# Optimization experiments

Hardware: AMD Instinct MI355X
Metric: run time of the kernel (lower is better)

## Reference

```python
import jax, jax.numpy as jnp
import numpy as np

N = 10000      # nodes
E = 320000     # edges
IN = 256       # in_dim == out_dim
H = 8          # heads
D = 32         # head_dim = in_dim // heads
CLAMP = 5.0
BN_EPS = 1e-5


def setup_inputs() -> dict:
    key = jax.random.key(0)
    ks = jax.random.split(key, 24)
    s = 0.05
    nrm = lambda k, shape, sc=s: (jax.random.normal(k, shape, jnp.float32) * sc)
    inp = {
        "x": nrm(ks[0], (N, IN), 1.0),
        "edge_attr": nrm(ks[1], (E, IN), 1.0),
        "log_deg": jax.random.uniform(ks[2], (N, 1), jnp.float32, 0.1, 3.0),
        "edge_index": jax.random.randint(ks[3], (2, E), 0, N, jnp.int32),
        # attention projections (stored [in, out]; x @ W + b)
        "Qw": nrm(ks[4], (IN, H * D)), "Qb": jnp.zeros((H * D,), jnp.float32),
        "Kw": nrm(ks[5], (IN, H * D)), "Kb": jnp.zeros((H * D,), jnp.float32),
        "Ew": nrm(ks[6], (IN, H * D * 2)), "Eb": jnp.zeros((H * D * 2,), jnp.float32),
        "Vw": nrm(ks[7], (IN, H * D)), "Vb": jnp.zeros((H * D,), jnp.float32),
        "Aw": nrm(ks[8], (D, H, 1)),
        "VeRow": nrm(ks[9], (D, H, D)),
        # layer params
        "deg_coef": nrm(ks[10], (1, H * D, 2)),
        "Now": nrm(ks[11], (H * D, IN)), "Nob": jnp.zeros((IN,), jnp.float32),
        "Eow": nrm(ks[12], (H * D, IN)), "Eob": jnp.zeros((IN,), jnp.float32),
        "bn1n_g": jnp.ones((IN,), jnp.float32), "bn1n_b": jnp.zeros((IN,), jnp.float32),
        "bn1e_g": jnp.ones((IN,), jnp.float32), "bn1e_b": jnp.zeros((IN,), jnp.float32),
        "f1w": nrm(ks[13], (IN, 2 * IN)), "f1b": jnp.zeros((2 * IN,), jnp.float32),
        "f2w": nrm(ks[14], (2 * IN, IN)), "f2b": jnp.zeros((IN,), jnp.float32),
        "bn2_g": jnp.ones((IN,), jnp.float32), "bn2_b": jnp.zeros((IN,), jnp.float32),
    }
    return inp


def _bn(x, g, b):
    # batch_norm with batch statistics (bn_no_runner=True => track_running_stats=False)
    mu = jnp.mean(x, axis=0)
    var = jnp.mean(jnp.square(x - mu), axis=0)  # biased, as torch BN
    return (x - mu) * jax.lax.rsqrt(var + BN_EPS) * g + b


def _attention(x, edge_attr, edge_index, Qw, Qb, Kw, Kb, Ew, Eb, Vw, Vb, Aw, VeRow):
    n = x.shape[0]
    src, dst = edge_index[0], edge_index[1]
    Qh = (x @ Qw + Qb).reshape(n, H, D)
    Kh = (x @ Kw + Kb).reshape(n, H, D)
    Vh = (x @ Vw + Vb).reshape(n, H, D)
    Ex = (edge_attr @ Ew + Eb).reshape(-1, H, 2 * D)
    score1 = Kh[src] + Qh[dst]                      # [E,H,D]
    s2 = Ex[:, :, :D] * Ex[:, :, D:]
    score2 = jnp.sign(s2) * jnp.sqrt(jnp.abs(s2))   # == sqrt(relu(s2)) - sqrt(relu(-s2))
    conn = jax.nn.relu(score1 + score2)             # [E,H,D] (attn act='relu')
    score = jnp.einsum('ehd,dhc->ehc', conn, Aw)    # [E,H,1]
    score = jnp.clip(score, -CLAMP, CLAMP)
    # segment softmax over destination nodes
    m = jax.ops.segment_max(score, dst, num_segments=n)
    e = jnp.exp(score - m[dst])
    ssum = jax.ops.segment_sum(e, dst, num_segments=n)
    attn = e / (ssum[dst] + 1e-16)                  # [E,H,1]
    msg = Vh[src] * attn
    Vo = Qh + jax.ops.segment_sum(msg, dst, num_segments=n)
    rowV = jax.ops.segment_sum(conn * attn, dst, num_segments=n)
    rowV = jnp.einsum('nhd,dhc->nhc', rowV, VeRow)
    Vo = Vo + rowV
    return Vo.reshape(n, H * D), conn.reshape(-1, H * D)


def reference(x, edge_attr, log_deg, edge_index, Qw, Qb, Kw, Kb, Ew, Eb, Vw, Vb,
              Aw, VeRow, deg_coef, Now, Nob, Eow, Eob, bn1n_g, bn1n_b,
              bn1e_g, bn1e_b, f1w, f1b, f2w, f2b, bn2_g, bn2_b):
    nh, eh = _attention(x, edge_attr, edge_index, Qw, Qb, Kw, Kb, Ew, Eb, Vw, Vb, Aw, VeRow)
    # degree scaler
    nh = nh * deg_coef[:, :, 0] + (nh * log_deg) * deg_coef[:, :, 1]
    nh = nh @ Now + Nob
    eh = eh @ Eow + Eob
    nh = x + nh
    eh = edge_attr + eh
    nh = _bn(nh, bn1n_g, bn1n_b)
    eh = _bn(eh, bn1e_g, bn1e_b)
    ffn = jax.nn.relu(nh @ f1w + f1b) @ f2w + f2b
    nh = _bn(nh + ffn, bn2_g, bn2_b)
    return nh, eh
```

## Files before the change

### kernel.cpp

```cpp
#include <hip/hip_runtime.h>

#define NN 10000
#define NE 320000

typedef float f4 __attribute__((ext_vector_type(4)));
typedef float f32x4 __attribute__((ext_vector_type(4)));
typedef short bf16x8 __attribute__((ext_vector_type(8)));

__device__ __forceinline__ unsigned short f2b(float f) {
  unsigned u = __float_as_uint(f);
  u += 0x7fff + ((u >> 16) & 1);
  return (unsigned short)(u >> 16);
}
__device__ __forceinline__ float b2f(unsigned short s) {
  return __uint_as_float(((unsigned)s) << 16);
}
__device__ __forceinline__ bf16x8 pack8(f4 a, f4 b) {
  bf16x8 r;
  r[0] = (short)f2b(a[0]); r[1] = (short)f2b(a[1]);
  r[2] = (short)f2b(a[2]); r[3] = (short)f2b(a[3]);
  r[4] = (short)f2b(b[0]); r[5] = (short)f2b(b[1]);
  r[6] = (short)f2b(b[2]); r[7] = (short)f2b(b[3]);
  return r;
}
__device__ __forceinline__ int swz(int row, int k) {
  return (row * 256) + (k ^ ((row & 7) << 3));
}

__global__ void castw_k(const float* __restrict__ in, unsigned short* __restrict__ out,
                        int K, int lg)
{
  int idx = blockIdx.x * 256 + threadIdx.x;
  if (idx >= (K << lg)) return;
  int n = idx & ((1 << lg) - 1), k = idx >> lg;
  out[(size_t)n * K + k] = f2b(in[idx]);
}

__global__ void cat3_k(const float* __restrict__ a, const float* __restrict__ b,
                       const float* __restrict__ c, float* __restrict__ o)
{
  int t = threadIdx.x;
  o[t] = a[t]; o[256 + t] = b[t]; o[512 + t] = c[t];
}

__global__ __launch_bounds__(256) void gemm_bf16_k(
    const float* __restrict__ A, const unsigned short* __restrict__ BT,
    const float* __restrict__ bias, const float* __restrict__ res,
    float* __restrict__ C, float* __restrict__ stats,
    int M, int K, int NT, int flags)
{
  __shared__ unsigned short Al[64][40];
  __shared__ unsigned short Bl[128][40];
  const int t = threadIdx.x;
  const int n0 = blockIdx.x * 128;
  const int m0 = blockIdx.y * 64;
  const int lane = t & 63, c = lane & 15, g = lane >> 4, w = t >> 6;
  f32x4 acc[8] = {};
  for (int k0 = 0; k0 < K; k0 += 32) {
    {
      int row = t >> 2, kk = (t & 3) * 8;
      f4 v0 = {0.f,0.f,0.f,0.f}, v1 = {0.f,0.f,0.f,0.f};
      if (m0 + row < M) {
        const f4* p = (const f4*)(A + (size_t)(m0 + row) * K + k0 + kk);
        v0 = p[0]; v1 = p[1];
      }
      __syncthreads();
      *(bf16x8*)&Al[row][kk] = pack8(v0, v1);
    }
    {
      int col = t >> 1, kk = (t & 1) * 16;
      const bf16x8* p = (const bf16x8*)(BT + (size_t)(n0 + col) * K + k0 + kk);
      *(bf16x8*)&Bl[col][kk] = p[0];
      *(bf16x8*)&Bl[col][kk + 8] = p[1];
    }
    __syncthreads();
    bf16x8 a = *(bf16x8*)&Al[w * 16 + c][g * 8];
#pragma unroll
    for (int nb = 0; nb < 8; nb++) {
      bf16x8 b = *(bf16x8*)&Bl[nb * 16 + c][g * 8];
      acc[nb] = __builtin_amdgcn_mfma_f32_16x16x32_bf16(a, b, acc[nb], 0, 0, 0);
    }
  }
  const int do_relu = flags & 1, do_stats = flags & 2;
#pragma unroll
  for (int nb = 0; nb < 8; nb++) {
    const int col = n0 + nb * 16 + c;
    const float bs = bias[col];
    float sn = 0.f, qn = 0.f;
#pragma unroll
    for (int r = 0; r < 4; r++) {
      int row = m0 + w * 16 + g * 4 + r;
      if (row < M) {
        float v = acc[nb][r] + bs;
        if (res) v += res[(size_t)row * NT + col];
        if (do_relu) v = fmaxf(v, 0.f);
        C[(size_t)row * NT + col] = v;
        sn += v; qn += v * v;
      }
    }
    if (do_stats) {
      sn += __shfl_xor(sn, 16); sn += __shfl_xor(sn, 32);
      qn += __shfl_xor(qn, 16); qn += __shfl_xor(qn, 32);
      if (g == 0) {
        atomicAdd(&stats[col], sn);
        atomicAdd(&stats[NT + col], qn);
      }
    }
  }
}

__global__ __launch_bounds__(256) void edge_conn_k(
    const float* __restrict__ EA, const unsigned short* __restrict__ EwT,
    const float* __restrict__ Eb, const float* __restrict__ QKVh,
    const int* __restrict__ ei, const float* __restrict__ Aw,
    float* __restrict__ connf, unsigned short* __restrict__ connb,
    float* __restrict__ score, int CB)
{
  __shared__ unsigned short Abuf[16384];
  __shared__ unsigned short Bbuf[16384];
  float* Exl = (float*)Bbuf;
  const int t = threadIdx.x;
  const int e0 = blockIdx.x * 64;
  const int lane = t & 63, c = lane & 15, g = lane >> 4, w = t >> 6;
#pragma unroll
  for (int it = 0; it < 8; it++) {
    int o = t + it * 256;
    int row = o >> 5, kk = (o & 31) * 8;
    const f4* p = (const f4*)(EA + (size_t)(e0 + row) * 256 + kk);
    f4 v0 = p[0], v1 = p[1];
    *(bf16x8*)&Abuf[swz(row, kk)] = pack8(v0, v1);
  }
  const int m2 = t >> 2, dg = t & 3;
  const int e = e0 + m2;
  const int src = ei[e], dst = ei[NE + e];
  for (int h = 0; h < 8; h++) {
    __syncthreads();
#pragma unroll
    for (int it = 0; it < 8; it++) {
      int o = t + it * 256;
      int row = o >> 5, kk = (o & 31) * 8;
      *(bf16x8*)&Bbuf[swz(row, kk)] =
          *(const bf16x8*)(EwT + (size_t)(h * 64 + row) * 256 + kk);
    }
    __syncthreads();
    f32x4 acc[4] = {};
#pragma unroll
    for (int ks = 0; ks < 8; ks++) {
      bf16x8 a = *(bf16x8*)&Abuf[swz(w * 16 + c, ks * 32 + g * 8)];
#pragma unroll
      for (int cb = 0; cb < 4; cb++) {
        bf16x8 b = *(bf16x8*)&Bbuf[swz(cb * 16 + c, ks * 32 + g * 8)];
        acc[cb] = __builtin_amdgcn_mfma_f32_16x16x32_bf16(a, b, acc[cb], 0, 0, 0);
      }
    }
    __syncthreads();
#pragma unroll
    for (int cb = 0; cb < 4; cb++) {
      float eb = Eb[h * 64 + cb * 16 + c];
#pragma unroll
      for (int r = 0; r < 4; r++)
        Exl[(w * 16 + g * 4 + r) * 68 + cb * 16 + c] = acc[cb][r] + eb;
    }
    __syncthreads();
    const int cb2 = h * 32 + dg * 8;
    const float* ex = Exl + m2 * 68;
    f4 x1a = *(const f4*)(ex + dg * 8);
    f4 x1b = *(const f4*)(ex + dg * 8 + 4);
    f4 x2a = *(const f4*)(ex + 32 + dg * 8);
    f4 x2b = *(const f4*)(ex + 32 + dg * 8 + 4);
    f4 k1 = *(const f4*)(QKVh + (size_t)src * 768 + 256 + cb2);
    f4 k2 = *(const f4*)(QKVh + (size_t)src * 768 + 256 + cb2 + 4);
    f4 q1 = *(const f4*)(QKVh + (size_t)dst * 768 + cb2);
    f4 q2 = *(const f4*)(QKVh + (size_t)dst * 768 + cb2 + 4);
    f4 c1, c2;
    float part = 0.f;
#pragma unroll
    for (int j = 0; j < 4; j++) {
      float s2 = x1a[j] * x2a[j];
      float v = copysignf(sqrtf(fabsf(s2)), s2) + k1[j] + q1[j];
      v = fmaxf(v, 0.f);
      c1[j] = v;
      part += v * Aw[(dg * 8 + j) * 8 + h];
      float s2b = x1b[j] * x2b[j];
      float vb = copysignf(sqrtf(fabsf(s2b)), s2b) + k2[j] + q2[j];
      vb = fmaxf(vb, 0.f);
      c2[j] = vb;
      part += vb * Aw[(dg * 8 + 4 + j) * 8 + h];
    }
    if (CB) {
      *(bf16x8*)(connb + (size_t)e * 256 + cb2) = pack8(c1, c2);
    } else {
      *(f4*)(connf + (size_t)e * 256 + cb2) = c1;
      *(f4*)(connf + (size_t)e * 256 + cb2 + 4) = c2;
    }
    part += __shfl_xor(part, 1);
    part += __shfl_xor(part, 2);
    if (dg == 0) score[(size_t)e * 8 + h] = fminf(fmaxf(part, -5.f), 5.f);
  }
}

__global__ void hist_k(const int* __restrict__ ei, int* __restrict__ cnt)
{
  int e = blockIdx.x * 256 + threadIdx.x;
  if (e < NE) atomicAdd(&cnt[ei[NE + e]], 1);
}

__global__ __launch_bounds__(256) void scan_k(const int* __restrict__ cnt, int* __restrict__ off)
{
  __shared__ int part[256];
  const int t = threadIdx.x;
  const int PER = 40;
  const int base = t * PER;
  int s = 0;
  for (int i = 0; i < PER; i++) {
    int b = base + i;
    if (b < NN) s += cnt[b];
  }
  part[t] = s;
  __syncthreads();
  for (int d = 1; d < 256; d <<= 1) {
    int v = (t >= d) ? part[t - d] : 0;
    __syncthreads();
    part[t] += v;
    __syncthreads();
  }
  int run = (t == 0) ? 0 : part[t - 1];
  for (int i = 0; i < PER; i++) {
    int b = base + i;
    if (b < NN) { off[b] = run; run += cnt[b]; }
  }
  if (t == 255) off[NN] = run;
}

__global__ void scat_k(const int* __restrict__ ei, const int* __restrict__ off,
                       int* __restrict__ cur, int* __restrict__ elist,
                       int* __restrict__ src_s)
{
  int e = blockIdx.x * 256 + threadIdx.x;
  if (e < NE) {
    int s = ei[e], d = ei[NE + e];
    int p = atomicAdd(&cur[d], 1);
    int j = off[d] + p;
    elist[j] = e;
    src_s[j] = s;
  }
}

__global__ __launch_bounds__(256) void node_agg_k(
    const int* __restrict__ off, const int* __restrict__ elist,
    const int* __restrict__ src_s, const float* __restrict__ score,
    const float* __restrict__ QKVh, const float* __restrict__ connf,
    const unsigned short* __restrict__ connb, int CB,
    const float* __restrict__ VeRow, const float* __restrict__ deg_coef,
    const float* __restrict__ log_deg, float* __restrict__ nh_a)
{
  const int n = blockIdx.x, t = threadIdx.x;
  const int h = t >> 5;
  __shared__ int eL[128];
  __shared__ int srcL[128];
  __shared__ float sS[1024];
  __shared__ float mS[8];
  __shared__ float rA[256];
  const int start = off[n];
  const int deg = off[n + 1] - start;
  float m = -1e30f, ssum = 0.f, vo = 0.f, ro = 0.f;
  for (int c0 = 0; c0 < deg; c0 += 128) {
    const int cn = min(128, deg - c0);
    __syncthreads();
    if (t < cn) {
      int jj = start + c0 + t;
      eL[t] = elist[jj];
      srcL[t] = src_s[jj];
    }
    __syncthreads();
    for (int i = t; i < cn * 8; i += 256) sS[i] = score[(size_t)eL[i >> 3] * 8 + (i & 7)];
    __syncthreads();
    float mc = -1e30f;
    for (int i = (t & 31); i < cn; i += 32) mc = fmaxf(mc, sS[i * 8 + h]);
    mc = fmaxf(mc, __shfl_xor(mc, 1));
    mc = fmaxf(mc, __shfl_xor(mc, 2));
    mc = fmaxf(mc, __shfl_xor(mc, 4));
    mc = fmaxf(mc, __shfl_xor(mc, 8));
    mc = fmaxf(mc, __shfl_xor(mc, 16));
    float nm = fmaxf(m, mc);
    if ((t & 31) == 0) mS[h] = nm;
    __syncthreads();
    for (int i = t; i < cn * 8; i += 256) sS[i] = __expf(sS[i] - mS[i & 7]);
    __syncthreads();
    float sc = __expf(m - nm);
    ssum *= sc; vo *= sc; ro *= sc;
    m = nm;
    int i = 0;
    if (CB) {
      for (; i + 4 <= cn; i += 4) {
        float w0 = sS[(i + 0) * 8 + h], w1 = sS[(i + 1) * 8 + h];
        float w2 = sS[(i + 2) * 8 + h], w3 = sS[(i + 3) * 8 + h];
        int s0 = srcL[i], s1 = srcL[i + 1], s2 = srcL[i + 2], s3 = srcL[i + 3];
        int f0 = eL[i], f1 = eL[i + 1], f2 = eL[i + 2], f3 = eL[i + 3];
        ssum += w0 + w1 + w2 + w3;
        vo = fmaf(w0, QKVh[(size_t)s0 * 768 + 512 + t], vo);
        vo = fmaf(w1, QKVh[(size_t)s1 * 768 + 512 + t], vo);
        vo = fmaf(w2, QKVh[(size_t)s2 * 768 + 512 + t], vo);
        vo = fmaf(w3, QKVh[(size_t)s3 * 768 + 512 + t], vo);
        ro = fmaf(w0, b2f(connb[(size_t)f0 * 256 + t]), ro);
        ro = fmaf(w1, b2f(connb[(size_t)f1 * 256 + t]), ro);
        ro = fmaf(w2, b2f(connb[(size_t)f2 * 256 + t]), ro);
        ro = fmaf(w3, b2f(connb[(size_t)f3 * 256 + t]), ro);
      }
      for (; i < cn; i++) {
        float w0 = sS[i * 8 + h];
        ssum += w0;
        vo = fmaf(w0, QKVh[(size_t)srcL[i] * 768 + 512 + t], vo);
        ro = fmaf(w0, b2f(connb[(size_t)eL[i] * 256 + t]), ro);
      }
    } else {
      for (; i + 4 <= cn; i += 4) {
        float w0 = sS[(i + 0) * 8 + h], w1 = sS[(i + 1) * 8 + h];
        float w2 = sS[(i + 2) * 8 + h], w3 = sS[(i + 3) * 8 + h];
        int s0 = srcL[i], s1 = srcL[i + 1], s2 = srcL[i + 2], s3 = srcL[i + 3];
        int f0 = eL[i], f1 = eL[i + 1], f2 = eL[i + 2], f3 = eL[i + 3];
        ssum += w0 + w1 + w2 + w3;
        vo = fmaf(w0, QKVh[(size_t)s0 * 768 + 512 + t], vo);
        vo = fmaf(w1, QKVh[(size_t)s1 * 768 + 512 + t], vo);
        vo = fmaf(w2, QKVh[(size_t)s2 * 768 + 512 + t], vo);
        vo = fmaf(w3, QKVh[(size_t)s3 * 768 + 512 + t], vo);
        ro = fmaf(w0, connf[(size_t)f0 * 256 + t], ro);
        ro = fmaf(w1, connf[(size_t)f1 * 256 + t], ro);
        ro = fmaf(w2, connf[(size_t)f2 * 256 + t], ro);
        ro = fmaf(w3, connf[(size_t)f3 * 256 + t], ro);
      }
      for (; i < cn; i++) {
        float w0 = sS[i * 8 + h];
        ssum += w0;
        vo = fmaf(w0, QKVh[(size_t)srcL[i] * 768 + 512 + t], vo);
        ro = fmaf(w0, connf[(size_t)eL[i] * 256 + t], ro);
      }
    }
  }
  const float inv = 1.f / (ssum + 1e-16f);
  vo *= inv;
  ro *= inv;
  __syncthreads();
  rA[t] = ro;
  __syncthreads();
  float acc = 0.f;
#pragma unroll
  for (int d = 0; d < 32; d++) acc = fmaf(rA[h * 32 + d], VeRow[d * 256 + t], acc);
  float v = QKVh[(size_t)n * 768 + t] + vo + acc;
  const float ld = log_deg[n];
  v = v * (deg_coef[2 * t] + ld * deg_coef[2 * t + 1]);
  nh_a[(size_t)n * 256 + t] = v;
}

__global__ __launch_bounds__(256) void eh_gemm_k(
    const unsigned short* __restrict__ EowT, const float* __restrict__ Eob,
    const float* __restrict__ EA, const unsigned short* __restrict__ connb, int CB,
    float* __restrict__ eh, float* __restrict__ stb)
{
  __shared__ unsigned short Al[64][264];
  __shared__ unsigned short Bl[256][40];
  __shared__ float lsum[256], lsq[256];
  const int t = threadIdx.x;
  const int e0 = blockIdx.x * 64;
  const int lane = t & 63, c = lane & 15, g = lane >> 4, w = t >> 6;
  lsum[t] = 0.f; lsq[t] = 0.f;
#pragma unroll
  for (int it = 0; it < 8; it++) {
    int o = t + it * 256;
    int row = o >> 5, kk = (o & 31) * 8;
    if (CB) {
      *(bf16x8*)&Al[row][kk] = *(const bf16x8*)(connb + (size_t)(e0 + row) * 256 + kk);
    } else {
      const f4* p = (const f4*)(eh + (size_t)(e0 + row) * 256 + kk);
      f4 v0 = p[0], v1 = p[1];
      *(bf16x8*)&Al[row][kk] = pack8(v0, v1);
    }
  }
  f32x4 acc[16] = {};
  for (int ks = 0; ks < 8; ks++) {
    __syncthreads();
#pragma unroll
    for (int it = 0; it < 4; it++) {
      int o = t + it * 256;
      int row = o >> 2, kk = (o & 3) * 8;
      *(bf16x8*)&Bl[row][kk] = *(const bf16x8*)(EowT + (size_t)row * 256 + ks * 32 + kk);
    }
    __syncthreads();
    bf16x8 a = *(bf16x8*)&Al[w * 16 + c][ks * 32 + g * 8];
#pragma unroll
    for (int nb = 0; nb < 16; nb++) {
      bf16x8 b = *(bf16x8*)&Bl[nb * 16 + c][g * 8];
      acc[nb] = __builtin_amdgcn_mfma_f32_16x16x32_bf16(a, b, acc[nb], 0, 0, 0);
    }
  }
#pragma unroll
  for (int nb = 0; nb < 16; nb++) {
    const int col = nb * 16 + c;
    const float eob = Eob[col];
    float sn = 0.f, qn = 0.f;
#pragma unroll
    for (int r = 0; r < 4; r++) {
      size_t row = e0 + w * 16 + g * 4 + r;
      float v = acc[nb][r] + eob + EA[row * 256 + col];
      eh[row * 256 + col] = v;
      sn += v; qn += v * v;
    }
    sn += __shfl_xor(sn, 16); sn += __shfl_xor(sn, 32);
    qn += __shfl_xor(qn, 16); qn += __shfl_xor(qn, 32);
    if (g == 0) { atomicAdd(&lsum[col], sn); atomicAdd(&lsq[col], qn); }
  }
  __syncthreads();
  float* dstb = stb + (size_t)(blockIdx.x & 63) * 512;
  atomicAdd(&dstb[t], lsum[t]);
  atomicAdd(&dstb[256 + t], lsq[t]);
}

__global__ void bn_fin_k(float* __restrict__ st, float invR)
{
  int t = threadIdx.x;
  float mean = st[t] * invR;
  float var = st[256 + t] * invR - mean * mean;
  st[t] = mean;
  st[256 + t] = rsqrtf(var + 1e-5f);
}

__global__ void bn_fin_banked_k(const float* __restrict__ banks, float* __restrict__ st,
                                float invR)
{
  int t = threadIdx.x;
  float s = 0.f, q = 0.f;
  for (int b = 0; b < 64; b++) {
    s += banks[(size_t)b * 512 + t];
    q += banks[(size_t)b * 512 + 256 + t];
  }
  float mean = s * invR;
  float var = q * invR - mean * mean;
  st[t] = mean;
  st[256 + t] = rsqrtf(var + 1e-5f);
}

__global__ void bn_apply_k(const float* __restrict__ X, float* __restrict__ Y,
                           const float* __restrict__ st, const float* __restrict__ g,
                           const float* __restrict__ b, long nvec)
{
  long i = (long)blockIdx.x * 256 + threadIdx.x;
  if (i >= nvec) return;
  int base = (int)(i & 63) * 4;
  f4 x = *(const f4*)(X + i * 4);
  f4 mn = *(const f4*)(st + base);
  f4 rs = *(const f4*)(st + 256 + base);
  f4 gg = *(const f4*)(g + base);
  f4 bb = *(const f4*)(b + base);
  f4 y;
#pragma unroll
  for (int j = 0; j < 4; j++) y[j] = (x[j] - mn[j]) * rs[j] * gg[j] + bb[j];
  *(f4*)(Y + i * 4) = y;
}

extern "C" void kernel_launch(void* const* d_in, const int* in_sizes, int n_in,
                              void* d_out, int out_size, void* d_ws, size_t ws_size,
                              hipStream_t stream)
{
  (void)in_sizes; (void)n_in; (void)out_size;
  const float* x        = (const float*)d_in[0];
  const float* edge_attr= (const float*)d_in[1];
  const float* log_deg  = (const float*)d_in[2];
  const int*   ei       = (const int*)d_in[3];
  const float* Qw = (const float*)d_in[4];  const float* Qb = (const float*)d_in[5];
  const float* Kw = (const float*)d_in[6];  const float* Kb = (const float*)d_in[7];
  const float* Ew = (const float*)d_in[8];  const float* Eb = (const float*)d_in[9];
  const float* Vw = (const float*)d_in[10]; const float* Vb = (const float*)d_in[11];
  const float* Aw = (const float*)d_in[12]; const float* VeRow = (const float*)d_in[13];
  const float* deg_coef = (const float*)d_in[14];
  const float* Now = (const float*)d_in[15]; const float* Nob = (const float*)d_in[16];
  const float* Eow = (const float*)d_in[17]; const float* Eob = (const float*)d_in[18];
  const float* bn1n_g = (const float*)d_in[19]; const float* bn1n_b = (const float*)d_in[20];
  const float* bn1e_g = (const float*)d_in[21]; const float* bn1e_b = (const float*)d_in[22];
  const float* f1w = (const float*)d_in[23]; const float* f1b = (const float*)d_in[24];
  const float* f2w = (const float*)d_in[25]; const float* f2b = (const float*)d_in[26];
  const float* bn2_g = (const float*)d_in[27]; const float* bn2_b = (const float*)d_in[28];

  float* out_nh = (float*)d_out;
  float* out_eh = out_nh + (size_t)NN * 256;

  float* ws     = (float*)d_ws;
  float* QKVh   = ws;
  float* score  = QKVh + (size_t)NN * 768;
  float* nh_a   = score + 2560000;
  float* nh2    = nh_a + 2560000;
  float* ffn1   = nh2 + 2560000;
  float* st1    = ffn1 + 5120000;
  float* st2    = st1 + 512;
  float* st3    = st2 + 512;
  float* stb    = st3 + 512;
  float* biasQKV= stb + 64 * 512;
  unsigned short* QwT = (unsigned short*)(biasQKV + 768);
  unsigned short* KwT = QwT + 65536;
  unsigned short* VwT = KwT + 65536;
  unsigned short* NowT= VwT + 65536;
  unsigned short* EowT= NowT + 65536;
  unsigned short* EwT = EowT + 65536;
  unsigned short* f1wT= EwT + 131072;
  unsigned short* f2wT= f1wT + 131072;
  int*   cnt    = (int*)(f2wT + 131072);
  int*   off    = cnt + NN;
  int*   cur    = off + NN + 1;
  int*   elist  = cur + NN;
  int*   src_s  = elist + NE;
  unsigned short* connb = (unsigned short*)(src_s + NE);
  size_t need = (size_t)((char*)(connb + (size_t)NE * 256) - (char*)d_ws);
  const int CB = (ws_size >= need) ? 1 : 0;

  hipMemsetAsync(cnt, 0, (size_t)NN * 4, stream);
  hipMemsetAsync(cur, 0, (size_t)NN * 4, stream);
  hipMemsetAsync(st1, 0, (size_t)2 * 512 * 4, stream);
  hipMemsetAsync(stb, 0, (size_t)64 * 512 * 4, stream);

  dim3 blk(256);

  castw_k<<<dim3(256), blk, 0, stream>>>(Qw, QwT, 256, 8);
  castw_k<<<dim3(256), blk, 0, stream>>>(Kw, KwT, 256, 8);
  castw_k<<<dim3(256), blk, 0, stream>>>(Vw, VwT, 256, 8);
  castw_k<<<dim3(256), blk, 0, stream>>>(Now, NowT, 256, 8);
  castw_k<<<dim3(256), blk, 0, stream>>>(Eow, EowT, 256, 8);
  castw_k<<<dim3(512), blk, 0, stream>>>(Ew, EwT, 256, 9);
  castw_k<<<dim3(512), blk, 0, stream>>>(f1w, f1wT, 256, 9);
  castw_k<<<dim3(512), blk, 0, stream>>>(f2w, f2wT, 512, 8);
  cat3_k<<<dim3(1), blk, 0, stream>>>(Qb, Kb, Vb, biasQKV);

  hist_k<<<dim3(NE / 256), blk, 0, stream>>>(ei, cnt);
  scan_k<<<dim3(1), blk, 0, stream>>>(cnt, off);
  scat_k<<<dim3(NE / 256), blk, 0, stream>>>(ei, off, cur, elist, src_s);

  gemm_bf16_k<<<dim3(6, 157), blk, 0, stream>>>(x, QwT, biasQKV, nullptr, QKVh, nullptr,
                                                NN, 256, 768, 0);

  edge_conn_k<<<dim3(NE / 64), blk, 0, stream>>>(edge_attr, EwT, Eb, QKVh, ei, Aw,
                                                 out_eh, connb, score, CB);

  node_agg_k<<<dim3(NN), blk, 0, stream>>>(off, elist, src_s, score, QKVh,
                                           out_eh, connb, CB,
                                           VeRow, deg_coef, log_deg, nh_a);

  eh_gemm_k<<<dim3(NE / 64), blk, 0, stream>>>(EowT, Eob, edge_attr, connb, CB,
                                               out_eh, stb);
  bn_fin_banked_k<<<dim3(1), blk, 0, stream>>>(stb, st3, 1.0f / NE);
  bn_apply_k<<<dim3(NE * 64 / 256), blk, 0, stream>>>(out_eh, out_eh, st3,
                                                      bn1e_g, bn1e_b, (long)NE * 64);

  gemm_bf16_k<<<dim3(2, 157), blk, 0, stream>>>(nh_a, NowT, Nob, x, out_nh, st1,
                                                NN, 256, 256, 2);
  bn_fin_k<<<dim3(1), blk, 0, stream>>>(st1, 1.0f / NN);
  bn_apply_k<<<dim3(NN * 64 / 256), blk, 0, stream>>>(out_nh, nh2, st1,
                                                      bn1n_g, bn1n_b, (long)NN * 64);
  gemm_bf16_k<<<dim3(4, 157), blk, 0, stream>>>(nh2, f1wT, f1b, nullptr, ffn1, nullptr,
                                                NN, 256, 512, 1);
  gemm_bf16_k<<<dim3(2, 157), blk, 0, stream>>>(ffn1, f2wT, f2b, nh2, out_nh, st2,
                                                NN, 512, 256, 2);
  bn_fin_k<<<dim3(1), blk, 0, stream>>>(st2, 1.0f / NN);
  bn_apply_k<<<dim3(NN * 64 / 256), blk, 0, stream>>>(out_nh, out_nh, st2,
                                                      bn2_g, bn2_b, (long)NN * 64);
}
```

Baseline: 1.020 ms.

## Store pre-BN edge output as bf16 and restructure edge_conn staging/prefetch

The edge GEMM epilogue now stages its pre-BatchNorm result in shared memory as bf16 and writes a bf16 intermediate buffer when the workspace is large enough. A new BN-apply kernel reads that bf16 buffer and writes fp32 output, which halves the bytes of the intermediate round trip. In edge_conn_k, the projected edge features are kept in a separate bf16 shared buffer so fewer barriers are needed, and the K/Q gathers for the next head are prefetched during the current one. The extra bf16 rounding of intermediates may add precision error, and the bf16 path needs a larger workspace.

```diff
diff --git a/kernel.cpp b/kernel.cpp
--- a/kernel.cpp
+++ b/kernel.cpp
@@ -118,7 +118,7 @@
 {
   __shared__ unsigned short Abuf[16384];
   __shared__ unsigned short Bbuf[16384];
-  float* Exl = (float*)Bbuf;
+  __shared__ unsigned short ExlB[64 * 72];
   const int t = threadIdx.x;
   const int e0 = blockIdx.x * 64;
   const int lane = t & 63, c = lane & 15, g = lane >> 4, w = t >> 6;
@@ -133,8 +133,14 @@
   const int m2 = t >> 2, dg = t & 3;
   const int e = e0 + m2;
   const int src = ei[e], dst = ei[NE + e];
+  const float* kbase = QKVh + (size_t)src * 768 + 256 + dg * 8;
+  const float* qbase = QKVh + (size_t)dst * 768 + dg * 8;
+  f4 k1 = *(const f4*)(kbase);
+  f4 k2 = *(const f4*)(kbase + 4);
+  f4 q1 = *(const f4*)(qbase);
+  f4 q2 = *(const f4*)(qbase + 4);
+  __syncthreads();
   for (int h = 0; h < 8; h++) {
-    __syncthreads();
 #pragma unroll
     for (int it = 0; it < 8; it++) {
       int o = t + it * 256;
@@ -153,49 +159,55 @@
         acc[cb] = __builtin_amdgcn_mfma_f32_16x16x32_bf16(a, b, acc[cb], 0, 0, 0);
       }
     }
-    __syncthreads();
 #pragma unroll
     for (int cb = 0; cb < 4; cb++) {
       float eb = Eb[h * 64 + cb * 16 + c];
 #pragma unroll
       for (int r = 0; r < 4; r++)
-        Exl[(w * 16 + g * 4 + r) * 68 + cb * 16 + c] = acc[cb][r] + eb;
-    }
-    __syncthreads();
-    const int cb2 = h * 32 + dg * 8;
-    const float* ex = Exl + m2 * 68;
-    f4 x1a = *(const f4*)(ex + dg * 8);
-    f4 x1b = *(const f4*)(ex + dg * 8 + 4);
-    f4 x2a = *(const f4*)(ex + 32 + dg * 8);
-    f4 x2b = *(const f4*)(ex + 32 + dg * 8 + 4);
-    f4 k1 = *(const f4*)(QKVh + (size_t)src * 768 + 256 + cb2);
-    f4 k2 = *(const f4*)(QKVh + (size_t)src * 768 + 256 + cb2 + 4);
-    f4 q1 = *(const f4*)(QKVh + (size_t)dst * 768 + cb2);
-    f4 q2 = *(const f4*)(QKVh + (size_t)dst * 768 + cb2 + 4);
-    f4 c1, c2;
-    float part = 0.f;
-#pragma unroll
-    for (int j = 0; j < 4; j++) {
-      float s2 = x1a[j] * x2a[j];
-      float v = copysignf(sqrtf(fabsf(s2)), s2) + k1[j] + q1[j];
-      v = fmaxf(v, 0.f);
-      c1[j] = v;
-      part += v * Aw[(dg * 8 + j) * 8 + h];
-      float s2b = x1b[j] * x2b[j];
-      float vb = copysignf(sqrtf(fabsf(s2b)), s2b) + k2[j] + q2[j];
-      vb = fmaxf(vb, 0.f);
-      c2[j] = vb;
-      part += vb * Aw[(dg * 8 + 4 + j) * 8 + h];
-    }
-    if (CB) {
-      *(bf16x8*)(connb + (size_t)e * 256 + cb2) = pack8(c1, c2);
-    } else {
-      *(f4*)(connf + (size_t)e * 256 + cb2) = c1;
-      *(f4*)(connf + (size_t)e * 256 + cb2 + 4) = c2;
-    }
-    part += __shfl_xor(part, 1);
-    part += __shfl_xor(part, 2);
-    if (dg == 0) score[(size_t)e * 8 + h] = fminf(fmaxf(part, -5.f), 5.f);
+        ExlB[(w * 16 + g * 4 + r) * 72 + cb * 16 + c] = f2b(acc[cb][r] + eb);
+    }
+    f4 nk1, nk2, nq1, nq2;
+    if (h < 7) {
+      nk1 = *(const f4*)(kbase + (h + 1) * 32);
+      nk2 = *(const f4*)(kbase + (h + 1) * 32 + 4);
+      nq1 = *(const f4*)(qbase + (h + 1) * 32);
+      nq2 = *(const f4*)(qbase + (h + 1) * 32 + 4);
+    }
+    {
+      bf16x8 x1 = *(bf16x8*)&ExlB[m2 * 72 + dg * 8];
+      bf16x8 x2 = *(bf16x8*)&ExlB[m2 * 72 + 32 + dg * 8];
+      const int cb2 = h * 32 + dg * 8;
+      f4 c1, c2;
+      float part = 0.f;
+#pragma unroll
+      for (int j = 0; j < 4; j++) {
+        float ex1 = b2f((unsigned short)x1[j]);
+        float ex2 = b2f((unsigned short)x2[j]);
+        float s2 = ex1 * ex2;
+        float v = copysignf(sqrtf(fabsf(s2)), s2) + k1[j] + q1[j];
+        v = fmaxf(v, 0.f);
+        c1[j] = v;
+        part += v * Aw[(dg * 8 + j) * 8 + h];
+        float ex1b = b2f((unsigned short)x1[j + 4]);
+        float ex2b = b2f((unsigned short)x2[j + 4]);
+        float s2b = ex1b * ex2b;
+        float vb = copysignf(sqrtf(fabsf(s2b)), s2b) + k2[j] + q2[j];
+        vb = fmaxf(vb, 0.f);
+        c2[j] = vb;
+        part += vb * Aw[(dg * 8 + 4 + j) * 8 + h];
+      }
+      if (CB) {
+        *(bf16x8*)(connb + (size_t)e * 256 + cb2) = pack8(c1, c2);
+      } else {
+        *(f4*)(connf + (size_t)e * 256 + cb2) = c1;
+        *(f4*)(connf + (size_t)e * 256 + cb2 + 4) = c2;
+      }
+      part += __shfl_xor(part, 1);
+      part += __shfl_xor(part, 2);
+      if (dg == 0) score[(size_t)e * 8 + h] = fminf(fmaxf(part, -5.f), 5.f);
+    }
+    if (h < 7) { k1 = nk1; k2 = nk2; q1 = nq1; q2 = nq2; }
+    __syncthreads();
   }
 }
 
@@ -355,7 +367,8 @@
 __global__ __launch_bounds__(256) void eh_gemm_k(
     const unsigned short* __restrict__ EowT, const float* __restrict__ Eob,
     const float* __restrict__ EA, const unsigned short* __restrict__ connb, int CB,
-    float* __restrict__ eh, float* __restrict__ stb)
+    float* __restrict__ eh, unsigned short* __restrict__ ehb, int EB,
+    float* __restrict__ stb)
 {
   __shared__ unsigned short Al[64][264];
   __shared__ unsigned short Bl[256][40];
@@ -393,6 +406,7 @@
       acc[nb] = __builtin_amdgcn_mfma_f32_16x16x32_bf16(a, b, acc[nb], 0, 0, 0);
     }
   }
+  if (EB) __syncthreads();
 #pragma unroll
   for (int nb = 0; nb < 16; nb++) {
     const int col = nb * 16 + c;
@@ -402,7 +416,8 @@
     for (int r = 0; r < 4; r++) {
       size_t row = e0 + w * 16 + g * 4 + r;
       float v = acc[nb][r] + eob + EA[row * 256 + col];
-      eh[row * 256 + col] = v;
+      if (EB) Al[w * 16 + g * 4 + r][col] = f2b(v);
+      else    eh[row * 256 + col] = v;
       sn += v; qn += v * v;
     }
     sn += __shfl_xor(sn, 16); sn += __shfl_xor(sn, 32);
@@ -410,6 +425,14 @@
     if (g == 0) { atomicAdd(&lsum[col], sn); atomicAdd(&lsq[col], qn); }
   }
   __syncthreads();
+  if (EB) {
+#pragma unroll
+    for (int it = 0; it < 8; it++) {
+      int o = t + it * 256;
+      int row = o >> 5, kk = (o & 31) * 8;
+      *(bf16x8*)(ehb + (size_t)(e0 + row) * 256 + kk) = *(bf16x8*)&Al[row][kk];
+    }
+  }
   float* dstb = stb + (size_t)(blockIdx.x & 63) * 512;
   atomicAdd(&dstb[t], lsum[t]);
   atomicAdd(&dstb[256 + t], lsq[t]);
@@ -455,6 +478,24 @@
 #pragma unroll
   for (int j = 0; j < 4; j++) y[j] = (x[j] - mn[j]) * rs[j] * gg[j] + bb[j];
   *(f4*)(Y + i * 4) = y;
+}
+
+__global__ void bn_apply_b_k(const unsigned short* __restrict__ X, float* __restrict__ Y,
+                             const float* __restrict__ st, const float* __restrict__ g,
+                             const float* __restrict__ b, long nvec8)
+{
+  long i = (long)blockIdx.x * 256 + threadIdx.x;
+  if (i >= nvec8) return;
+  int base = (int)(i & 31) * 8;
+  bf16x8 x = *(const bf16x8*)(X + i * 8);
+  f4 y0, y1;
+#pragma unroll
+  for (int j = 0; j < 4; j++) {
+    y0[j] = (b2f((unsigned short)x[j]) - st[base + j]) * st[256 + base + j] * g[base + j] + b[base + j];
+    y1[j] = (b2f((unsigned short)x[j + 4]) - st[base + 4 + j]) * st[256 + base + 4 + j] * g[base + 4 + j] + b[base + 4 + j];
+  }
+  *(f4*)(Y + i * 8) = y0;
+  *(f4*)(Y + i * 8 + 4) = y1;
 }
 
 extern "C" void kernel_launch(void* const* d_in, const int* in_sizes, int n_in,
@@ -508,8 +549,11 @@
   int*   elist  = cur + NN;
   int*   src_s  = elist + NE;
   unsigned short* connb = (unsigned short*)(src_s + NE);
-  size_t need = (size_t)((char*)(connb + (size_t)NE * 256) - (char*)d_ws);
-  const int CB = (ws_size >= need) ? 1 : 0;
+  unsigned short* ehb   = connb + (size_t)NE * 256;
+  size_t need1 = (size_t)((char*)ehb - (char*)d_ws);
+  size_t need2 = (size_t)((char*)(ehb + (size_t)NE * 256) - (char*)d_ws);
+  const int CB = (ws_size >= need1) ? 1 : 0;
+  const int EB = (CB && ws_size >= need2) ? 1 : 0;
 
   hipMemsetAsync(cnt, 0, (size_t)NN * 4, stream);
   hipMemsetAsync(cur, 0, (size_t)NN * 4, stream);
@@ -543,10 +587,15 @@
                                            VeRow, deg_coef, log_deg, nh_a);
 
   eh_gemm_k<<<dim3(NE / 64), blk, 0, stream>>>(EowT, Eob, edge_attr, connb, CB,
-                                               out_eh, stb);
+                                               out_eh, ehb, EB, stb);
   bn_fin_banked_k<<<dim3(1), blk, 0, stream>>>(stb, st3, 1.0f / NE);
-  bn_apply_k<<<dim3(NE * 64 / 256), blk, 0, stream>>>(out_eh, out_eh, st3,
-                                                      bn1e_g, bn1e_b, (long)NE * 64);
+  if (EB) {
+    bn_apply_b_k<<<dim3(NE * 32 / 256), blk, 0, stream>>>(ehb, out_eh, st3,
+                                                          bn1e_g, bn1e_b, (long)NE * 32);
+  } else {
+    bn_apply_k<<<dim3(NE * 64 / 256), blk, 0, stream>>>(out_eh, out_eh, st3,
+                                                        bn1e_g, bn1e_b, (long)NE * 64);
+  }
 
   gemm_bf16_k<<<dim3(2, 157), blk, 0, stream>>>(nh_a, NowT, Nob, x, out_nh, st1,
                                                 NN, 256, 256, 2);
```

Result: slower. 1.164 ms (+14.2%).
